# Optimization experiments

Hardware: AMD Instinct MI355X
Metric: run time of the kernel (lower is better)

## Reference

```python
import jax, jax.numpy as jnp
import numpy as np
import math

D_MODEL = 1024
D_HIDDEN = 64
H = 16
B = 2
N = 2048


def softmax_one(x, axis=-1):
    # exp(x - max) / (1 + sum(exp(x - max))) -- matches the torch code exactly
    m = jnp.max(x, axis=axis, keepdims=True)
    e = jnp.exp(x - m)
    return e / (1.0 + jnp.sum(e, axis=axis, keepdims=True))


def setup_inputs() -> dict:
    key = jax.random.key(0)
    ks = jax.random.split(key, 8)
    queries = jax.random.normal(ks[0], (B, N, D_MODEL), dtype=jnp.float32)
    keys = jax.random.normal(ks[1], (B, N, D_MODEL), dtype=jnp.float32)
    values = jax.random.normal(ks[2], (B, N, D_MODEL), dtype=jnp.float32)
    std = 0.02
    Wq = std * jax.random.normal(ks[3], (H * D_HIDDEN, D_MODEL), dtype=jnp.float32)
    Wk = std * jax.random.normal(ks[4], (H * D_HIDDEN, D_MODEL), dtype=jnp.float32)
    Wv = std * jax.random.normal(ks[5], (H * D_HIDDEN, D_MODEL), dtype=jnp.float32)
    Wo = std * jax.random.normal(ks[6], (D_MODEL, H * D_HIDDEN), dtype=jnp.float32)
    bq = jnp.zeros((H * D_HIDDEN,), jnp.float32)
    bk = jnp.zeros((H * D_HIDDEN,), jnp.float32)
    bv = jnp.zeros((H * D_HIDDEN,), jnp.float32)
    bo = jnp.zeros((D_MODEL,), jnp.float32)
    return {"queries": queries, "keys": keys, "values": values,
            "Wq": Wq, "bq": bq, "Wk": Wk, "bk": bk,
            "Wv": Wv, "bv": bv, "Wo": Wo, "bo": bo}


def reference(queries, keys, values, Wq, bq, Wk, bk, Wv, bv, Wo, bo):
    b_s, nq, _ = queries.shape
    nk = keys.shape[1]
    # projections: (b, n, h*dh) -> (b, h, n, dh)
    q = (queries @ Wq.T + bq).reshape(b_s, nq, H, D_HIDDEN).transpose(0, 2, 1, 3)
    k = (keys @ Wk.T + bk).reshape(b_s, nk, H, D_HIDDEN).transpose(0, 2, 1, 3)
    v = (values @ Wv.T + bv).reshape(b_s, nk, H, D_HIDDEN).transpose(0, 2, 1, 3)
    scale = 1.0 / math.sqrt(D_HIDDEN)
    scores = jnp.einsum('bhqd,bhkd->bhqk', q, k) * scale  # (b, h, nq, nk)
    attn = softmax_one(scores, axis=-1)  # dropout disabled (eval)
    out = jnp.einsum('bhqk,bhkd->bhqd', attn, v)  # (b, h, nq, dh)
    out = out.transpose(0, 2, 1, 3).reshape(b_s, nq, H * D_HIDDEN)
    out = out @ Wo.T + bo
    present = jnp.stack((k, v))  # (2, b, h, nk, dh)
    return (out, present)
```

## Files before the change

kernel.cpp:

```cpp
#include <hip/hip_runtime.h>
#include <math.h>

#define D_MODEL 1024
#define DH 64
#define NH 16
#define BS 2
#define SEQ 2048
#define MTOT (BS*SEQ)

typedef _Float16 f16x8 __attribute__((ext_vector_type(8)));
typedef _Float16 f16x4 __attribute__((ext_vector_type(4)));
typedef float f32x4 __attribute__((ext_vector_type(4)));
typedef unsigned int u32;

__device__ __forceinline__ void load_lds16(const void* g, void* l) {
    __builtin_amdgcn_global_load_lds(
        (const __attribute__((address_space(1))) u32*)g,
        (__attribute__((address_space(3))) u32*)l, 16, 0, 0);
}

__global__ __launch_bounds__(256) void convert_all_kernel(
    const float* __restrict__ s0, const float* __restrict__ s1, const float* __restrict__ s2,
    const float* __restrict__ s3, const float* __restrict__ s4, const float* __restrict__ s5,
    const float* __restrict__ s6,
    _Float16* __restrict__ d0, _Float16* __restrict__ d1, _Float16* __restrict__ d2,
    _Float16* __restrict__ d3, _Float16* __restrict__ d4, _Float16* __restrict__ d5,
    _Float16* __restrict__ d6, int nX, int nW)
{
    int y = blockIdx.y;
    const float* s; _Float16* d; int n;
    switch (y) {
        case 0: s = s0; d = d0; n = nX; break;
        case 1: s = s1; d = d1; n = nX; break;
        case 2: s = s2; d = d2; n = nX; break;
        case 3: s = s3; d = d3; n = nW; break;
        case 4: s = s4; d = d4; n = nW; break;
        case 5: s = s5; d = d5; n = nW; break;
        default: s = s6; d = d6; n = nW; break;
    }
    int i = (blockIdx.x * 256 + threadIdx.x) * 8;
    if (i < n) {
        float4 a = *(const float4*)(s + i);
        float4 b = *(const float4*)(s + i + 4);
        f16x8 o;
        o[0] = (_Float16)a.x; o[1] = (_Float16)a.y; o[2] = (_Float16)a.z; o[3] = (_Float16)a.w;
        o[4] = (_Float16)b.x; o[5] = (_Float16)b.y; o[6] = (_Float16)b.z; o[7] = (_Float16)b.w;
        *(f16x8*)(d + i) = o;
    }
}

__global__ __launch_bounds__(256) void qkv_proj_kernel(
    const _Float16* __restrict__ Xq, const _Float16* __restrict__ Xk, const _Float16* __restrict__ Xv,
    const _Float16* __restrict__ Wq, const _Float16* __restrict__ Wk, const _Float16* __restrict__ Wv,
    const float* __restrict__ bq, const float* __restrict__ bk, const float* __restrict__ bv,
    _Float16* __restrict__ qh, _Float16* __restrict__ kh, _Float16* __restrict__ vt,
    float* __restrict__ outp)
{
    __shared__ __align__(16) _Float16 ldsA[2][128][64];
    __shared__ __align__(16) _Float16 ldsB[2][128][64];

    const int jb = blockIdx.x >> 5;
    const int ib = blockIdx.x & 31;
    const int id = jb >> 3;
    const int col0 = (jb & 7) << 7;
    const int row0 = ib << 7;

    const _Float16* X  = (id == 0) ? Xq : (id == 1) ? Xk : Xv;
    const _Float16* W  = (id == 0) ? Wq : (id == 1) ? Wk : Wv;
    const float* bias  = (id == 0) ? bq : (id == 1) ? bk : bv;

    const int tid = threadIdx.x;
    const int w = tid >> 6, lane = tid & 63;
    const int quad = lane >> 4, l16 = lane & 15;
    const int wm = (w >> 1) << 6, wn = (w & 1) << 6;

    const int r_loc = lane >> 3;
    const int sg = ((lane & 7) ^ r_loc) << 3;

    const f32x4 zero = {0.f, 0.f, 0.f, 0.f};
    f32x4 acc[4][4];
#pragma unroll
    for (int i = 0; i < 4; i++)
#pragma unroll
        for (int j = 0; j < 4; j++) acc[i][j] = zero;

#pragma unroll
    for (int i = 0; i < 4; i++) {
        int r = i * 32 + w * 8;
        load_lds16(X + (size_t)(row0 + r + r_loc) * D_MODEL + sg, &ldsA[0][r][0]);
        load_lds16(W + (size_t)(col0 + r + r_loc) * D_MODEL + sg, &ldsB[0][r][0]);
    }

    for (int t = 0; t < D_MODEL / 64; t++) {
        const int cur = t & 1;

        __builtin_amdgcn_s_barrier();

        if (t + 1 < D_MODEL / 64) {
            const int k1 = (t + 1) << 6;
#pragma unroll
            for (int i = 0; i < 4; i++) {
                int r = i * 32 + w * 8;
                load_lds16(X + (size_t)(row0 + r + r_loc) * D_MODEL + k1 + sg, &ldsA[cur ^ 1][r][0]);
                load_lds16(W + (size_t)(col0 + r + r_loc) * D_MODEL + k1 + sg, &ldsB[cur ^ 1][r][0]);
            }
            asm volatile("s_waitcnt vmcnt(8)" ::: "memory");
        } else {
            asm volatile("s_waitcnt vmcnt(0)" ::: "memory");
        }

        __builtin_amdgcn_s_barrier();

#pragma unroll
        for (int kk = 0; kk < 2; kk++) {
            f16x8 af[4], bfr[4];
#pragma unroll
            for (int mi = 0; mi < 4; mi++)
                af[mi]  = *(const f16x8*)&ldsA[cur][wm + mi*16 + l16][(((kk<<2) + quad) ^ (l16 & 7)) << 3];
#pragma unroll
            for (int ni = 0; ni < 4; ni++)
                bfr[ni] = *(const f16x8*)&ldsB[cur][wn + ni*16 + l16][(((kk<<2) + quad) ^ (l16 & 7)) << 3];
#pragma unroll
            for (int mi = 0; mi < 4; mi++)
#pragma unroll
                for (int ni = 0; ni < 4; ni++)
                    acc[mi][ni] = __builtin_amdgcn_mfma_f32_16x16x32_f16(af[mi], bfr[ni], acc[mi][ni], 0, 0, 0);
        }
    }

    const size_t OUT0 = (size_t)MTOT * D_MODEL;
    const size_t PRES = (size_t)BS * NH * SEQ * DH;
#pragma unroll
    for (int ni = 0; ni < 4; ni++) {
        int gn = col0 + wn + ni * 16 + l16;
        float bias_v = bias[gn];
        int h = gn >> 6, d = gn & 63;
#pragma unroll
        for (int mi = 0; mi < 4; mi++) {
            int gm0 = row0 + wm + mi * 16 + quad * 4;
            int b = gm0 >> 11, n0 = gm0 & 2047;
            size_t bh = (size_t)(b * NH + h);
            if (id == 0) {
#pragma unroll
                for (int r = 0; r < 4; r++) {
                    float val = acc[mi][ni][r] + bias_v;
                    qh[(bh * SEQ + n0 + r) * DH + d] = (_Float16)val;
                }
            } else if (id == 1) {
#pragma unroll
                for (int r = 0; r < 4; r++) {
                    float val = acc[mi][ni][r] + bias_v;
                    size_t idx = (bh * SEQ + n0 + r) * DH + d;
                    outp[OUT0 + idx] = val;
                    kh[idx] = (_Float16)val;
                }
            } else {
                f16x4 o;
#pragma unroll
                for (int r = 0; r < 4; r++) {
                    float val = acc[mi][ni][r] + bias_v;
                    outp[OUT0 + PRES + (bh * SEQ + n0 + r) * DH + d] = val;
                    o[r] = (_Float16)val;
                }
                *(f16x4*)(vt + (bh * DH + d) * SEQ + n0) = o;
            }
        }
    }
}

__global__ __launch_bounds__(512) void attn_kernel(
    const _Float16* __restrict__ qh, const _Float16* __restrict__ kh,
    const _Float16* __restrict__ vt, _Float16* __restrict__ aout)
{
    __shared__ __align__(16) _Float16 Kt[2][64][76];
    __shared__ __align__(16) _Float16 Vt[2][64][76];

    const int bh = blockIdx.x & 31;
    const int qt = blockIdx.x >> 5;
    const int b = bh >> 4, h = bh & 15;
    const int tid = threadIdx.x;
    const int w = tid >> 6, lane = tid & 63;
    const int quad = lane >> 4, l16 = lane & 15;
    const int qr0 = qt * 128 + w * 16;

    const _Float16* Qb = qh + (size_t)bh * SEQ * DH;
    const _Float16* Kb = kh + (size_t)bh * SEQ * DH;
    const _Float16* Vb = vt + (size_t)bh * DH * SEQ;

    const float QSCALE = 0.125f * 1.44269504f;
    f16x8 aq[2];
#pragma unroll
    for (int ks = 0; ks < 2; ks++) {
        f16x8 t = *(const f16x8*)(Qb + (size_t)(qr0 + l16) * DH + ks * 32 + quad * 8);
#pragma unroll
        for (int j = 0; j < 8; j++) t[j] = (_Float16)((float)t[j] * QSCALE);
        aq[ks] = t;
    }

    const int sr = tid >> 3, sc = (tid & 7) << 3;

    *(f16x8*)&Kt[0][sr][sc] = *(const f16x8*)(Kb + (size_t)sr * DH + sc);
    *(f16x8*)&Vt[0][sr][sc] = *(const f16x8*)(Vb + (size_t)sr * SEQ + sc);
    __syncthreads();

    float m2 = -INFINITY, lsum = 0.f;
    const f32x4 zero = {0.f, 0.f, 0.f, 0.f};
    f32x4 accO[4];
#pragma unroll
    for (int db = 0; db < 4; db++) accO[db] = zero;

    for (int t = 0; t < SEQ / 64; t++) {
        const int cur = t & 1;
        const int kc = t * 64;

        f16x8 kr, vr;
        if (t + 1 < SEQ / 64) {
            kr = *(const f16x8*)(Kb + (size_t)(kc + 64 + sr) * DH + sc);
            vr = *(const f16x8*)(Vb + (size_t)sr * SEQ + kc + 64 + sc);
        }

        f32x4 sT[4];
#pragma unroll
        for (int nb = 0; nb < 4; nb++) sT[nb] = zero;
#pragma unroll
        for (int ks = 0; ks < 2; ks++)
#pragma unroll
            for (int nb = 0; nb < 4; nb++) {
                f16x8 kf = *(const f16x8*)&Kt[cur][nb*16 + l16][ks*32 + quad*8];
                sT[nb] = __builtin_amdgcn_mfma_f32_16x16x32_f16(kf, aq[ks], sT[nb], 0, 0, 0);
            }

        f16x4 pf[4];
#pragma unroll
        for (int nb = 0; nb < 4; nb++)
#pragma unroll
            for (int r = 0; r < 4; r++) {
                float s = sT[nb][r];
                m2 = fmaxf(m2, s);
                float e = __builtin_amdgcn_exp2f(s);
                lsum += e;
                pf[nb][r] = (_Float16)e;
            }

#pragma unroll
        for (int db = 0; db < 4; db++)
#pragma unroll
            for (int nb = 0; nb < 4; nb++) {
                f16x4 vf = *(const f16x4*)&Vt[cur][db*16 + l16][nb*16 + quad*4];
                accO[db] = __builtin_amdgcn_mfma_f32_16x16x16f16(vf, pf[nb], accO[db], 0, 0, 0);
            }

        if (t + 1 < SEQ / 64) {
            *(f16x8*)&Kt[cur ^ 1][sr][sc] = kr;
            *(f16x8*)&Vt[cur ^ 1][sr][sc] = vr;
        }
        __syncthreads();
    }

    m2 = fmaxf(m2, __shfl_xor(m2, 16));
    m2 = fmaxf(m2, __shfl_xor(m2, 32));
    lsum += __shfl_xor(lsum, 16);
    lsum += __shfl_xor(lsum, 32);

    const float inv = 1.f / (__builtin_amdgcn_exp2f(m2) + lsum);
    const int q = qr0 + l16;
    _Float16* orow = aout + ((size_t)b * SEQ + q) * D_MODEL + h * DH + quad * 4;
#pragma unroll
    for (int db = 0; db < 4; db++) {
        f16x4 o;
#pragma unroll
        for (int r = 0; r < 4; r++) o[r] = (_Float16)(accO[db][r] * inv);
        *(f16x4*)(orow + db * 16) = o;
    }
}

__global__ __launch_bounds__(256) void out_proj_kernel(
    const _Float16* __restrict__ aout, const _Float16* __restrict__ Wo,
    const float* __restrict__ bo, float* __restrict__ outp)
{
    __shared__ __align__(16) _Float16 ldsA[2][64][64];
    __shared__ __align__(16) _Float16 ldsB[2][128][64];

    const int jb = blockIdx.x >> 6;
    const int ib = blockIdx.x & 63;
    const int col0 = jb << 7, row0 = ib << 6;
    const int tid = threadIdx.x;
    const int w = tid >> 6, lane = tid & 63;
    const int quad = lane >> 4, l16 = lane & 15;
    const int wm = (w >> 1) << 5, wn = (w & 1) << 6;

    const int r_loc = lane >> 3;
    const int sg = ((lane & 7) ^ r_loc) << 3;

    const f32x4 zero = {0.f, 0.f, 0.f, 0.f};
    f32x4 acc[2][4];
#pragma unroll
    for (int i = 0; i < 2; i++)
#pragma unroll
        for (int j = 0; j < 4; j++) acc[i][j] = zero;

#pragma unroll
    for (int i = 0; i < 2; i++) {
        int r = i * 32 + w * 8;
        load_lds16(aout + (size_t)(row0 + r + r_loc) * D_MODEL + sg, &ldsA[0][r][0]);
    }
#pragma unroll
    for (int i = 0; i < 4; i++) {
        int r = i * 32 + w * 8;
        load_lds16(Wo + (size_t)(col0 + r + r_loc) * D_MODEL + sg, &ldsB[0][r][0]);
    }

    for (int t = 0; t < D_MODEL / 64; t++) {
        const int cur = t & 1;

        __builtin_amdgcn_s_barrier();

        if (t + 1 < D_MODEL / 64) {
            const int k1 = (t + 1) << 6;
#pragma unroll
            for (int i = 0; i < 2; i++) {
                int r = i * 32 + w * 8;
                load_lds16(aout + (size_t)(row0 + r + r_loc) * D_MODEL + k1 + sg, &ldsA[cur ^ 1][r][0]);
            }
#pragma unroll
            for (int i = 0; i < 4; i++) {
                int r = i * 32 + w * 8;
                load_lds16(Wo + (size_t)(col0 + r + r_loc) * D_MODEL + k1 + sg, &ldsB[cur ^ 1][r][0]);
            }
            asm volatile("s_waitcnt vmcnt(6)" ::: "memory");
        } else {
            asm volatile("s_waitcnt vmcnt(0)" ::: "memory");
        }

        __builtin_amdgcn_s_barrier();

#pragma unroll
        for (int kk = 0; kk < 2; kk++) {
            f16x8 af[2], bfr[4];
#pragma unroll
            for (int mi = 0; mi < 2; mi++)
                af[mi]  = *(const f16x8*)&ldsA[cur][wm + mi*16 + l16][(((kk<<2) + quad) ^ (l16 & 7)) << 3];
#pragma unroll
            for (int ni = 0; ni < 4; ni++)
                bfr[ni] = *(const f16x8*)&ldsB[cur][wn + ni*16 + l16][(((kk<<2) + quad) ^ (l16 & 7)) << 3];
#pragma unroll
            for (int mi = 0; mi < 2; mi++)
#pragma unroll
                for (int ni = 0; ni < 4; ni++)
                    acc[mi][ni] = __builtin_amdgcn_mfma_f32_16x16x32_f16(af[mi], bfr[ni], acc[mi][ni], 0, 0, 0);
        }
    }

#pragma unroll
    for (int ni = 0; ni < 4; ni++) {
        int gn = col0 + wn + ni * 16 + l16;
        float bias_v = bo[gn];
#pragma unroll
        for (int mi = 0; mi < 2; mi++)
#pragma unroll
            for (int r = 0; r < 4; r++) {
                int gm = row0 + wm + mi * 16 + quad * 4 + r;
                outp[(size_t)gm * D_MODEL + gn] = acc[mi][ni][r] + bias_v;
            }
    }
}

extern "C" void kernel_launch(void* const* d_in, const int* in_sizes, int n_in,
                              void* d_out, int out_size, void* d_ws, size_t ws_size,
                              hipStream_t stream)
{
    const float* queries = (const float*)d_in[0];
    const float* keys    = (const float*)d_in[1];
    const float* values  = (const float*)d_in[2];
    const float* Wq = (const float*)d_in[3];
    const float* bq = (const float*)d_in[4];
    const float* Wk = (const float*)d_in[5];
    const float* bk = (const float*)d_in[6];
    const float* Wv = (const float*)d_in[7];
    const float* bv = (const float*)d_in[8];
    const float* Wo = (const float*)d_in[9];
    const float* bo = (const float*)d_in[10];
    float* outp = (float*)d_out;

    const size_t NELT = (size_t)BS * NH * SEQ * DH;
    const size_t XN   = (size_t)MTOT * D_MODEL;
    const size_t WN   = (size_t)D_MODEL * D_MODEL;
    _Float16* qh   = (_Float16*)d_ws;
    _Float16* kh   = qh + NELT;
    _Float16* vt   = kh + NELT;
    _Float16* aout = vt + NELT;
    _Float16* Xfq  = aout + NELT;
    _Float16* Xfk  = Xfq + XN;
    _Float16* Xfv  = Xfk + XN;
    _Float16* Wfq  = Xfv + XN;
    _Float16* Wfk  = Wfq + WN;
    _Float16* Wfv  = Wfk + WN;
    _Float16* Wfo  = Wfv + WN;

    convert_all_kernel<<<dim3((int)(XN/2048), 7), dim3(256), 0, stream>>>(
        queries, keys, values, Wq, Wk, Wv, Wo,
        Xfq, Xfk, Xfv, Wfq, Wfk, Wfv, Wfo, (int)XN, (int)WN);

    qkv_proj_kernel<<<dim3(768), dim3(256), 0, stream>>>(
        Xfq, Xfk, Xfv, Wfq, Wfk, Wfv, bq, bk, bv, qh, kh, vt, outp);
    attn_kernel<<<dim3(512), dim3(512), 0, stream>>>(qh, kh, vt, aout);
    out_proj_kernel<<<dim3(512), dim3(256), 0, stream>>>(aout, Wfo, bo, outp);
}
```

Measured before the change: 233.7 us.

## Process two query row tiles per wave in attention kernel with 256 threads

The attention kernel now uses 4 waves per block, each handling 32 query rows (two 16-row MFMA tiles), instead of 8 waves with 16 rows each. Each K/V fragment read from LDS feeds two MFMAs, halving LDS read traffic per FLOP, and each thread now stages two rows of the K/V tile. This raises register pressure (double accumulators, scores and Q fragments) and halves the waves per block, which may reduce occupancy and latency hiding.

```diff
diff --git a/kernel.cpp b/kernel.cpp
--- a/kernel.cpp
+++ b/kernel.cpp
@@ -168,7 +168,7 @@
     }
 }
 
-__global__ __launch_bounds__(512) void attn_kernel(
+__global__ __launch_bounds__(256) void attn_kernel(
     const _Float16* __restrict__ qh, const _Float16* __restrict__ kh,
     const _Float16* __restrict__ vt, _Float16* __restrict__ aout)
 {
@@ -181,96 +181,123 @@
     const int tid = threadIdx.x;
     const int w = tid >> 6, lane = tid & 63;
     const int quad = lane >> 4, l16 = lane & 15;
-    const int qr0 = qt * 128 + w * 16;
+    const int qr0 = qt * 128 + w * 32;
 
     const _Float16* Qb = qh + (size_t)bh * SEQ * DH;
     const _Float16* Kb = kh + (size_t)bh * SEQ * DH;
     const _Float16* Vb = vt + (size_t)bh * DH * SEQ;
 
     const float QSCALE = 0.125f * 1.44269504f;
-    f16x8 aq[2];
-#pragma unroll
-    for (int ks = 0; ks < 2; ks++) {
-        f16x8 t = *(const f16x8*)(Qb + (size_t)(qr0 + l16) * DH + ks * 32 + quad * 8);
-#pragma unroll
-        for (int j = 0; j < 8; j++) t[j] = (_Float16)((float)t[j] * QSCALE);
-        aq[ks] = t;
-    }
+    f16x8 aq[2][2];
+#pragma unroll
+    for (int m = 0; m < 2; m++)
+#pragma unroll
+        for (int ks = 0; ks < 2; ks++) {
+            f16x8 t = *(const f16x8*)(Qb + (size_t)(qr0 + m*16 + l16) * DH + ks * 32 + quad * 8);
+#pragma unroll
+            for (int j = 0; j < 8; j++) t[j] = (_Float16)((float)t[j] * QSCALE);
+            aq[m][ks] = t;
+        }
 
     const int sr = tid >> 3, sc = (tid & 7) << 3;
 
-    *(f16x8*)&Kt[0][sr][sc] = *(const f16x8*)(Kb + (size_t)sr * DH + sc);
-    *(f16x8*)&Vt[0][sr][sc] = *(const f16x8*)(Vb + (size_t)sr * SEQ + sc);
+#pragma unroll
+    for (int rr = 0; rr < 2; rr++) {
+        *(f16x8*)&Kt[0][rr*32 + sr][sc] = *(const f16x8*)(Kb + (size_t)(rr*32 + sr) * DH + sc);
+        *(f16x8*)&Vt[0][rr*32 + sr][sc] = *(const f16x8*)(Vb + (size_t)(rr*32 + sr) * SEQ + sc);
+    }
     __syncthreads();
 
-    float m2 = -INFINITY, lsum = 0.f;
+    float m2[2] = {-INFINITY, -INFINITY};
+    float lsum[2] = {0.f, 0.f};
     const f32x4 zero = {0.f, 0.f, 0.f, 0.f};
-    f32x4 accO[4];
-#pragma unroll
-    for (int db = 0; db < 4; db++) accO[db] = zero;
+    f32x4 accO[2][4];
+#pragma unroll
+    for (int m = 0; m < 2; m++)
+#pragma unroll
+        for (int db = 0; db < 4; db++) accO[m][db] = zero;
 
     for (int t = 0; t < SEQ / 64; t++) {
         const int cur = t & 1;
         const int kc = t * 64;
 
-        f16x8 kr, vr;
+        f16x8 kr[2], vr[2];
         if (t + 1 < SEQ / 64) {
-            kr = *(const f16x8*)(Kb + (size_t)(kc + 64 + sr) * DH + sc);
-            vr = *(const f16x8*)(Vb + (size_t)sr * SEQ + kc + 64 + sc);
-        }
-
-        f32x4 sT[4];
-#pragma unroll
-        for (int nb = 0; nb < 4; nb++) sT[nb] = zero;
+#pragma unroll
+            for (int rr = 0; rr < 2; rr++) {
+                kr[rr] = *(const f16x8*)(Kb + (size_t)(kc + 64 + rr*32 + sr) * DH + sc);
+                vr[rr] = *(const f16x8*)(Vb + (size_t)(rr*32 + sr) * SEQ + kc + 64 + sc);
+            }
+        }
+
+        f32x4 sT[2][4];
+#pragma unroll
+        for (int m = 0; m < 2; m++)
+#pragma unroll
+            for (int nb = 0; nb < 4; nb++) sT[m][nb] = zero;
 #pragma unroll
         for (int ks = 0; ks < 2; ks++)
 #pragma unroll
             for (int nb = 0; nb < 4; nb++) {
                 f16x8 kf = *(const f16x8*)&Kt[cur][nb*16 + l16][ks*32 + quad*8];
-                sT[nb] = __builtin_amdgcn_mfma_f32_16x16x32_f16(kf, aq[ks], sT[nb], 0, 0, 0);
-            }
-
-        f16x4 pf[4];
-#pragma unroll
-        for (int nb = 0; nb < 4; nb++)
-#pragma unroll
-            for (int r = 0; r < 4; r++) {
-                float s = sT[nb][r];
-                m2 = fmaxf(m2, s);
-                float e = __builtin_amdgcn_exp2f(s);
-                lsum += e;
-                pf[nb][r] = (_Float16)e;
-            }
+#pragma unroll
+                for (int m = 0; m < 2; m++)
+                    sT[m][nb] = __builtin_amdgcn_mfma_f32_16x16x32_f16(kf, aq[m][ks], sT[m][nb], 0, 0, 0);
+            }
+
+        f16x4 pf[2][4];
+#pragma unroll
+        for (int m = 0; m < 2; m++)
+#pragma unroll
+            for (int nb = 0; nb < 4; nb++)
+#pragma unroll
+                for (int r = 0; r < 4; r++) {
+                    float s = sT[m][nb][r];
+                    m2[m] = fmaxf(m2[m], s);
+                    float e = __builtin_amdgcn_exp2f(s);
+                    lsum[m] += e;
+                    pf[m][nb][r] = (_Float16)e;
+                }
 
 #pragma unroll
         for (int db = 0; db < 4; db++)
 #pragma unroll
             for (int nb = 0; nb < 4; nb++) {
                 f16x4 vf = *(const f16x4*)&Vt[cur][db*16 + l16][nb*16 + quad*4];
-                accO[db] = __builtin_amdgcn_mfma_f32_16x16x16f16(vf, pf[nb], accO[db], 0, 0, 0);
+#pragma unroll
+                for (int m = 0; m < 2; m++)
+                    accO[m][db] = __builtin_amdgcn_mfma_f32_16x16x16f16(vf, pf[m][nb], accO[m][db], 0, 0, 0);
             }
 
         if (t + 1 < SEQ / 64) {
-            *(f16x8*)&Kt[cur ^ 1][sr][sc] = kr;
-            *(f16x8*)&Vt[cur ^ 1][sr][sc] = vr;
+#pragma unroll
+            for (int rr = 0; rr < 2; rr++) {
+                *(f16x8*)&Kt[cur ^ 1][rr*32 + sr][sc] = kr[rr];
+                *(f16x8*)&Vt[cur ^ 1][rr*32 + sr][sc] = vr[rr];
+            }
         }
         __syncthreads();
     }
 
-    m2 = fmaxf(m2, __shfl_xor(m2, 16));
-    m2 = fmaxf(m2, __shfl_xor(m2, 32));
-    lsum += __shfl_xor(lsum, 16);
-    lsum += __shfl_xor(lsum, 32);
-
-    const float inv = 1.f / (__builtin_amdgcn_exp2f(m2) + lsum);
-    const int q = qr0 + l16;
-    _Float16* orow = aout + ((size_t)b * SEQ + q) * D_MODEL + h * DH + quad * 4;
-#pragma unroll
-    for (int db = 0; db < 4; db++) {
-        f16x4 o;
-#pragma unroll
-        for (int r = 0; r < 4; r++) o[r] = (_Float16)(accO[db][r] * inv);
-        *(f16x4*)(orow + db * 16) = o;
+#pragma unroll
+    for (int m = 0; m < 2; m++) {
+        float mm = m2[m];
+        mm = fmaxf(mm, __shfl_xor(mm, 16));
+        mm = fmaxf(mm, __shfl_xor(mm, 32));
+        float ls = lsum[m];
+        ls += __shfl_xor(ls, 16);
+        ls += __shfl_xor(ls, 32);
+
+        const float inv = 1.f / (__builtin_amdgcn_exp2f(mm) + ls);
+        const int q = qr0 + m*16 + l16;
+        _Float16* orow = aout + ((size_t)b * SEQ + q) * D_MODEL + h * DH + quad * 4;
+#pragma unroll
+        for (int db = 0; db < 4; db++) {
+            f16x4 o;
+#pragma unroll
+            for (int r = 0; r < 4; r++) o[r] = (_Float16)(accO[m][db][r] * inv);
+            *(f16x4*)(orow + db * 16) = o;
+        }
     }
 }
 
@@ -403,6 +430,6 @@
 
     qkv_proj_kernel<<<dim3(768), dim3(256), 0, stream>>>(
         Xfq, Xfk, Xfv, Wfq, Wfk, Wfv, bq, bk, bv, qh, kh, vt, outp);
-    attn_kernel<<<dim3(512), dim3(512), 0, stream>>>(qh, kh, vt, aout);
+    attn_kernel<<<dim3(512), dim3(256), 0, stream>>>(qh, kh, vt, aout);
     out_proj_kernel<<<dim3(512), dim3(256), 0, stream>>>(aout, Wfo, bo, outp);
 }
```

Result: slower. 241.8 us (+3.4%).
